# Optimization experiments

Measured on AMD Instinct MI355X. Metric: run time of the kernel, lower is better.

## Reference

```python
import jax, jax.numpy as jnp
import numpy as np

EPS = 1e-12  # matches F.normalize eps

def _l2norm(x):
    n = jnp.sqrt(jnp.sum(x * x, axis=-1, keepdims=True))
    return x / jnp.maximum(n, EPS)

def setup_inputs() -> dict:
    key = jax.random.key(0)
    k1, k2, k3, k4 = jax.random.split(key, 4)
    Bq, Lq, H = 32, 32, 768
    ppq = 8
    Bd, Ld = Bq * ppq, 512
    dim = 128
    q_hidden = jax.random.normal(k1, (Bq, Lq, H), dtype=jnp.float32)
    d_hidden = jax.random.normal(k2, (Bd, Ld, H), dtype=jnp.float32)
    W = jax.random.normal(k3, (dim, H), dtype=jnp.float32) * (1.0 / np.sqrt(H))
    d_mask = jax.random.randint(k4, (Bd, Ld), 0, 2).astype(bool)
    d_mask = d_mask.at[:, 0].set(True)  # guarantee >=1 valid token per doc
    return {"q_hidden": q_hidden, "d_hidden": d_hidden, "W": W,
            "d_mask": d_mask, "ppq": ppq}

def reference(q_hidden, d_hidden, W, d_mask, ppq):
    # linear projection (no bias) + L2 normalize, as in query()/doc()
    q = _l2norm(jnp.einsum('bqh,dh->bqd', q_hidden, W))        # [Bq, Lq, dim]
    d = _l2norm(jnp.einsum('bkh,dh->bkd', d_hidden, W))        # [Bd, Ld, dim]
    d = d * d_mask[..., None].astype(d.dtype)                  # zero masked tokens
    qd = jnp.repeat(q, ppq, axis=0)                            # [Bd, Lq, dim]
    sim = jnp.einsum('bqd,bkd->bqk', qd, d)                    # cosine MaxSim scores
    sim = jnp.where(d_mask[:, None, :], sim, -jnp.inf)         # mask doc tokens
    return jnp.sum(jnp.max(sim, axis=-1), axis=-1)             # [Bd]
```

## Files before the change

kernel.cpp:

```cpp
#include <hip/hip_runtime.h>
#include <math.h>

#define H    768
#define NT   24
#define DIM  128
#define LQ   32
#define LD   512
#define BM   256
#define EPSF 1e-12f

typedef _Float16 f16x8 __attribute__((ext_vector_type(8)));
typedef _Float16 f16x4 __attribute__((ext_vector_type(4)));
typedef float    f32x4 __attribute__((ext_vector_type(4)));

static __device__ __forceinline__ unsigned short h2u(_Float16 h) {
    return __builtin_bit_cast(unsigned short, h);
}

#define GLOAD_LDS16(g, l) __builtin_amdgcn_global_load_lds(                    \
    (const __attribute__((address_space(1))) unsigned int*)(const void*)(g),   \
    (__attribute__((address_space(3))) unsigned int*)(void*)(l), 16, 0, 0)

__global__ __launch_bounds__(256) void wconv_kernel(
    const float* __restrict__ W, unsigned short* __restrict__ wsW,
    float* __restrict__ WT)
{
    const int ks  = blockIdx.x;
    const int tid = threadIdx.x;
    #pragma unroll 4
    for (int i = 0; i < 16; ++i) {
        const int idx = tid + i * 256;
        const int row = idx >> 5, col = idx & 31;
        const float x = W[(size_t)row * H + ks * 32 + col];
        const _Float16 hi = (_Float16)x;
        const _Float16 lo = (_Float16)(x - (float)hi);
        const int colS = (((col >> 3) ^ ((row >> 1) & 3)) << 3) | (col & 7);
        wsW[(((size_t)ks * 2 + 0) * 128 + row) * 32 + colS] = h2u(hi);
        wsW[(((size_t)ks * 2 + 1) * 128 + row) * 32 + colS] = h2u(lo);
        WT[((size_t)ks * 32 + col) * DIM + row] = x;
    }
}

__global__ __launch_bounds__(128) void qproj_kernel(
    const float* __restrict__ qh, const float* __restrict__ WT,
    unsigned short* __restrict__ qn)
{
    const int blk = blockIdx.x;
    const int tid = threadIdx.x;
    __shared__ float rows[4][H];
    __shared__ float red[128];

    const float4* src = (const float4*)(qh + (size_t)blk * 4 * H);
    float4*       dst = (float4*)&rows[0][0];
    for (int i = tid; i < 4 * H / 4; i += 128) dst[i] = src[i];
    __syncthreads();

    float acc[4] = {0.f, 0.f, 0.f, 0.f};
    #pragma unroll 8
    for (int h = 0; h < H; ++h) {
        const float wv = WT[(size_t)h * DIM + tid];
        acc[0] += wv * rows[0][h];
        acc[1] += wv * rows[1][h];
        acc[2] += wv * rows[2][h];
        acc[3] += wv * rows[3][h];
    }
    #pragma unroll
    for (int j = 0; j < 4; ++j) {
        red[tid] = acc[j] * acc[j];
        __syncthreads();
        for (int s = 64; s > 0; s >>= 1) {
            if (tid < s) red[tid] += red[tid + s];
            __syncthreads();
        }
        const float inv = 1.0f / fmaxf(sqrtf(red[0]), EPSF);
        qn[((size_t)blk * 4 + j) * DIM + tid] = h2u((_Float16)(acc[j] * inv));
        __syncthreads();
    }
}

struct Smem {
    union {
        struct {
            unsigned short A[2][BM][32];
            unsigned short Wt[2][2][128][32];
        } g;
        unsigned short C[BM][DIM];
    } u;
    float         pnorm[2][BM];
    unsigned char mk[BM];
    float         pmax[LQ][8];
};

__global__ __launch_bounds__(512, 4) void docgemm_kernel(
    const float* __restrict__ dh, const unsigned short* __restrict__ wsW,
    const int* __restrict__ dmask, const unsigned short* __restrict__ qn,
    float* __restrict__ part, const int* __restrict__ ppq_p)
{
    __shared__ Smem sm;
    const int blk = blockIdx.x;
    const int b   = blk >> 1;
    const int c   = blk & 1;
    const int tid = threadIdx.x;
    const int w   = tid >> 6;
    const int wm  = w >> 1, wn = w & 1;
    const int l   = tid & 63;
    const int g   = l >> 4;
    const int r15 = l & 15;
    const int ppq = ppq_p[0];

    const int r0   = tid >> 3;
    const int seg0 = tid & 7;
    const int aswz = (r0 >> 1) & 3;
    const int coli = (((seg0 >> 1) ^ aswz) << 3) | ((seg0 & 1) << 2);

    const float* Abase = dh + ((size_t)b * LD + (size_t)c * BM) * H;

    f32x4 acc[4][4];
    #pragma unroll
    for (int m = 0; m < 4; ++m)
        #pragma unroll
        for (int n = 0; n < 4; ++n)
            acc[m][n] = (f32x4){0.f, 0.f, 0.f, 0.f};

    float4 avA[4];

    {
        const char* wt   = (const char*)wsW;
        char*       wdst = (char*)&sm.u.g.Wt[0][0][0][0];
        GLOAD_LDS16(wt + tid * 16,        wdst + (w * 64) * 16);
        GLOAD_LDS16(wt + 8192 + tid * 16, wdst + 8192 + (w * 64) * 16);
        __builtin_amdgcn_sched_barrier(0);
        #pragma unroll
        for (int i = 0; i < 4; ++i)
            avA[i] = *(const float4*)(Abase + (size_t)(r0 + i * 64) * H + seg0 * 4);
        #pragma unroll
        for (int i = 0; i < 4; ++i) {
            const int row = r0 + i * 64;
            f16x4 h;
            h[0] = (_Float16)avA[i].x; h[1] = (_Float16)avA[i].y;
            h[2] = (_Float16)avA[i].z; h[3] = (_Float16)avA[i].w;
            *(f16x4*)&sm.u.g.A[0][row][coli] = h;
        }
        #pragma unroll
        for (int i = 0; i < 4; ++i)
            avA[i] = *(const float4*)(Abase + (size_t)(r0 + i * 64) * H + 32 + seg0 * 4);
        asm volatile("s_waitcnt vmcnt(4) lgkmcnt(0)" ::: "memory");
        __builtin_amdgcn_sched_barrier(0);
        __builtin_amdgcn_s_barrier();
        __builtin_amdgcn_sched_barrier(0);
    }

    for (int t = 0; t < NT; ++t) {
        const int cur = t & 1, nxt = cur ^ 1;

        if (t + 1 < NT) {
            const char* wt   = (const char*)wsW + (size_t)(t + 1) * 16384;
            char*       wdst = (char*)&sm.u.g.Wt[nxt][0][0][0];
            GLOAD_LDS16(wt + tid * 16,        wdst + (w * 64) * 16);
            GLOAD_LDS16(wt + 8192 + tid * 16, wdst + 8192 + (w * 64) * 16);
        }
        __builtin_amdgcn_sched_barrier(0);

        f16x8 ah[4];
        #pragma unroll
        for (int m = 0; m < 4; ++m) {
            const int row = wm * 64 + m * 16 + r15;
            const int sl  = (g ^ ((row >> 1) & 3)) * 8;
            ah[m] = *(const f16x8*)&sm.u.g.A[cur][row][sl];
        }
        __builtin_amdgcn_s_setprio(1);
        #pragma unroll
        for (int n = 0; n < 4; ++n) {
            const int row = wn * 64 + n * 16 + r15;
            const int sl  = (g ^ ((row >> 1) & 3)) * 8;
            f16x8 bh = *(const f16x8*)&sm.u.g.Wt[cur][0][row][sl];
            f16x8 bl = *(const f16x8*)&sm.u.g.Wt[cur][1][row][sl];
            #pragma unroll
            for (int m = 0; m < 4; ++m)
                acc[m][n] = __builtin_amdgcn_mfma_f32_16x16x32_f16(ah[m], bh, acc[m][n], 0, 0, 0);
            #pragma unroll
            for (int m = 0; m < 4; ++m)
                acc[m][n] = __builtin_amdgcn_mfma_f32_16x16x32_f16(ah[m], bl, acc[m][n], 0, 0, 0);
        }
        __builtin_amdgcn_s_setprio(0);

        if (t + 1 < NT) {
            #pragma unroll
            for (int i = 0; i < 4; ++i) {
                const int row = r0 + i * 64;
                f16x4 h;
                h[0] = (_Float16)avA[i].x; h[1] = (_Float16)avA[i].y;
                h[2] = (_Float16)avA[i].z; h[3] = (_Float16)avA[i].w;
                *(f16x4*)&sm.u.g.A[nxt][row][coli] = h;
            }
        }
        if (t + 2 < NT) {
            const int k0n = (t + 2) * 32;
            #pragma unroll
            for (int i = 0; i < 4; ++i)
                avA[i] = *(const float4*)(Abase + (size_t)(r0 + i * 64) * H + k0n + seg0 * 4);
        }

        if (t + 2 < NT) {
            asm volatile("s_waitcnt vmcnt(4) lgkmcnt(0)" ::: "memory");
        } else {
            asm volatile("s_waitcnt vmcnt(0) lgkmcnt(0)" ::: "memory");
        }
        __builtin_amdgcn_sched_barrier(0);
        __builtin_amdgcn_s_barrier();
        __builtin_amdgcn_sched_barrier(0);
    }

    #pragma unroll
    for (int m = 0; m < 4; ++m) {
        const int tokb = wm * 64 + m * 16 + g * 4;
        #pragma unroll
        for (int n = 0; n < 4; ++n) {
            const int dim = wn * 64 + n * 16 + r15;
            #pragma unroll
            for (int r = 0; r < 4; ++r) {
                const int tok  = tokb + r;
                const int slot = (dim >> 3) ^ (tok & 7);
                sm.u.C[tok][slot * 8 + (dim & 7)] = h2u((_Float16)acc[m][n][r]);
            }
        }
    }
    #pragma unroll
    for (int m = 0; m < 4; ++m) {
        #pragma unroll
        for (int r = 0; r < 4; ++r) {
            float s = 0.f;
            #pragma unroll
            for (int n = 0; n < 4; ++n) s += acc[m][n][r] * acc[m][n][r];
            s += __shfl_xor(s, 1); s += __shfl_xor(s, 2);
            s += __shfl_xor(s, 4); s += __shfl_xor(s, 8);
            if (r15 == 0) sm.pnorm[wn][wm * 64 + m * 16 + g * 4 + r] = s;
        }
    }
    if (tid < BM) sm.mk[tid] = (unsigned char)(dmask[(size_t)b * LD + c * BM + tid] != 0);
    __syncthreads();

    const unsigned short* qb = qn + (size_t)(b / ppq) * LQ * DIM;
    const int t0 = w * 32 + r15, t1 = t0 + 16;
    const float inv0 = 1.0f / fmaxf(sqrtf(sm.pnorm[0][t0] + sm.pnorm[1][t0]), EPSF);
    const float inv1 = 1.0f / fmaxf(sqrtf(sm.pnorm[0][t1] + sm.pnorm[1][t1]), EPSF);

    f32x4 sacc[2][2];
    #pragma unroll
    for (int m = 0; m < 2; ++m)
        #pragma unroll
        for (int n = 0; n < 2; ++n)
            sacc[m][n] = (f32x4){0.f, 0.f, 0.f, 0.f};
    #pragma unroll
    for (int ks = 0; ks < 4; ++ks) {
        f16x8 qa[2], cb[2];
        #pragma unroll
        for (int m = 0; m < 2; ++m)
            qa[m] = *(const f16x8*)(qb + (size_t)(m * 16 + r15) * DIM + ks * 32 + g * 8);
        #pragma unroll
        for (int n = 0; n < 2; ++n) {
            const int row  = w * 32 + n * 16 + r15;
            const int slot = (ks * 4 + g) ^ (row & 7);
            cb[n] = *(const f16x8*)&sm.u.C[row][slot * 8];
        }
        #pragma unroll
        for (int m = 0; m < 2; ++m)
            #pragma unroll
            for (int n = 0; n < 2; ++n)
                sacc[m][n] = __builtin_amdgcn_mfma_f32_16x16x32_f16(qa[m], cb[n], sacc[m][n], 0, 0, 0);
    }

    const int m0 = sm.mk[t0], m1 = sm.mk[t1];
    #pragma unroll
    for (int m = 0; m < 2; ++m) {
        #pragma unroll
        for (int r = 0; r < 4; ++r) {
            float v0 = m0 ? sacc[m][0][r] * inv0 : -INFINITY;
            float v1 = m1 ? sacc[m][1][r] * inv1 : -INFINITY;
            float vmax = fmaxf(v0, v1);
            vmax = fmaxf(vmax, __shfl_xor(vmax, 1));
            vmax = fmaxf(vmax, __shfl_xor(vmax, 2));
            vmax = fmaxf(vmax, __shfl_xor(vmax, 4));
            vmax = fmaxf(vmax, __shfl_xor(vmax, 8));
            if (r15 == 0) sm.pmax[m * 16 + g * 4 + r][w] = vmax;
        }
    }
    __syncthreads();
    if (tid < LQ) {
        float mv = sm.pmax[tid][0];
        #pragma unroll
        for (int j = 1; j < 8; ++j) mv = fmaxf(mv, sm.pmax[tid][j]);
        part[(size_t)blk * 32 + tid] = mv;
    }
}

__global__ __launch_bounds__(64) void final_kernel(
    const float* __restrict__ part, float* __restrict__ out)
{
    const int b = blockIdx.x;
    const int q = threadIdx.x & 31;
    const float* p = part + (size_t)b * 64;
    float m = fmaxf(p[q], p[32 + q]);
    #pragma unroll
    for (int off = 1; off < 32; off <<= 1) m += __shfl_xor(m, off);
    if (threadIdx.x == 0) out[b] = m;
}

extern "C" void kernel_launch(void* const* d_in, const int* in_sizes, int n_in,
                              void* d_out, int out_size, void* d_ws, size_t ws_size,
                              hipStream_t stream) {
    const float* qh    = (const float*)d_in[0];
    const float* dh    = (const float*)d_in[1];
    const float* W     = (const float*)d_in[2];
    const int*   dmask = (const int*)d_in[3];
    const int*   ppq   = (const int*)d_in[4];
    float*       out   = (float*)d_out;

    unsigned short* wsW  = (unsigned short*)d_ws;
    float*          WT   = (float*)((char*)d_ws + 393216);
    unsigned short* qn   = (unsigned short*)((char*)d_ws + 786432);
    float*          part = (float*)((char*)d_ws + 1048576);

    const int nq = in_sizes[0] / H;
    const int Bd = out_size;

    wconv_kernel<<<NT, 256, 0, stream>>>(W, wsW, WT);
    qproj_kernel<<<nq / 4, 128, 0, stream>>>(qh, WT, qn);
    docgemm_kernel<<<Bd * 2, 512, 0, stream>>>(dh, wsW, dmask, qn, part, ppq);
    final_kernel<<<Bd, 64, 0, stream>>>(part, out);
}
```

Baseline: 147.9 us.

## Drop the fp16 low-part correction for W and halve the doc tile

W is now stored as a single fp16 value instead of an fp16 hi/lo split. This halves the W staging buffer, the LDS B reads and the MFMA count per k-step. The doc GEMM tile also shrinks from 256 to 128 rows with 256 threads per block, so four blocks per document instead of two and more blocks in flight. The final reduction now combines four partial maxima per query token. The cost is lower projection precision, since the W rounding error is no longer compensated.

```diff
diff --git a/kernel.cpp b/kernel.cpp
--- a/kernel.cpp
+++ b/kernel.cpp
@@ -6,7 +6,7 @@
 #define DIM  128
 #define LQ   32
 #define LD   512
-#define BM   256
+#define BM   128
 #define EPSF 1e-12f
 
 typedef _Float16 f16x8 __attribute__((ext_vector_type(8)));
@@ -32,11 +32,8 @@
         const int idx = tid + i * 256;
         const int row = idx >> 5, col = idx & 31;
         const float x = W[(size_t)row * H + ks * 32 + col];
-        const _Float16 hi = (_Float16)x;
-        const _Float16 lo = (_Float16)(x - (float)hi);
         const int colS = (((col >> 3) ^ ((row >> 1) & 3)) << 3) | (col & 7);
-        wsW[(((size_t)ks * 2 + 0) * 128 + row) * 32 + colS] = h2u(hi);
-        wsW[(((size_t)ks * 2 + 1) * 128 + row) * 32 + colS] = h2u(lo);
+        wsW[((size_t)ks * 128 + row) * 32 + colS] = h2u((_Float16)x);
         WT[((size_t)ks * 32 + col) * DIM + row] = x;
     }
 }
@@ -82,24 +79,24 @@
     union {
         struct {
             unsigned short A[2][BM][32];
-            unsigned short Wt[2][2][128][32];
+            unsigned short Wt[2][128][32];
         } g;
         unsigned short C[BM][DIM];
     } u;
     float         pnorm[2][BM];
     unsigned char mk[BM];
-    float         pmax[LQ][8];
+    float         pmax[LQ][4];
 };
 
-__global__ __launch_bounds__(512, 4) void docgemm_kernel(
+__global__ __launch_bounds__(256, 4) void docgemm_kernel(
     const float* __restrict__ dh, const unsigned short* __restrict__ wsW,
     const int* __restrict__ dmask, const unsigned short* __restrict__ qn,
     float* __restrict__ part, const int* __restrict__ ppq_p)
 {
     __shared__ Smem sm;
     const int blk = blockIdx.x;
-    const int b   = blk >> 1;
-    const int c   = blk & 1;
+    const int b   = blk >> 2;
+    const int c   = blk & 3;
     const int tid = threadIdx.x;
     const int w   = tid >> 6;
     const int wm  = w >> 1, wn = w & 1;
@@ -126,16 +123,16 @@
 
     {
         const char* wt   = (const char*)wsW;
-        char*       wdst = (char*)&sm.u.g.Wt[0][0][0][0];
-        GLOAD_LDS16(wt + tid * 16,        wdst + (w * 64) * 16);
-        GLOAD_LDS16(wt + 8192 + tid * 16, wdst + 8192 + (w * 64) * 16);
+        char*       wdst = (char*)&sm.u.g.Wt[0][0][0];
+        GLOAD_LDS16(wt + tid * 16,        wdst + w * 1024);
+        GLOAD_LDS16(wt + 4096 + tid * 16, wdst + 4096 + w * 1024);
         __builtin_amdgcn_sched_barrier(0);
         #pragma unroll
         for (int i = 0; i < 4; ++i)
-            avA[i] = *(const float4*)(Abase + (size_t)(r0 + i * 64) * H + seg0 * 4);
+            avA[i] = *(const float4*)(Abase + (size_t)(r0 + i * 32) * H + seg0 * 4);
         #pragma unroll
         for (int i = 0; i < 4; ++i) {
-            const int row = r0 + i * 64;
+            const int row = r0 + i * 32;
             f16x4 h;
             h[0] = (_Float16)avA[i].x; h[1] = (_Float16)avA[i].y;
             h[2] = (_Float16)avA[i].z; h[3] = (_Float16)avA[i].w;
@@ -143,7 +140,7 @@
         }
         #pragma unroll
         for (int i = 0; i < 4; ++i)
-            avA[i] = *(const float4*)(Abase + (size_t)(r0 + i * 64) * H + 32 + seg0 * 4);
+            avA[i] = *(const float4*)(Abase + (size_t)(r0 + i * 32) * H + 32 + seg0 * 4);
         asm volatile("s_waitcnt vmcnt(4) lgkmcnt(0)" ::: "memory");
         __builtin_amdgcn_sched_barrier(0);
         __builtin_amdgcn_s_barrier();
@@ -154,10 +151,10 @@
         const int cur = t & 1, nxt = cur ^ 1;
 
         if (t + 1 < NT) {
-            const char* wt   = (const char*)wsW + (size_t)(t + 1) * 16384;
-            char*       wdst = (char*)&sm.u.g.Wt[nxt][0][0][0];
-            GLOAD_LDS16(wt + tid * 16,        wdst + (w * 64) * 16);
-            GLOAD_LDS16(wt + 8192 + tid * 16, wdst + 8192 + (w * 64) * 16);
+            const char* wt   = (const char*)wsW + (size_t)(t + 1) * 8192;
+            char*       wdst = (char*)&sm.u.g.Wt[nxt][0][0];
+            GLOAD_LDS16(wt + tid * 16,        wdst + w * 1024);
+            GLOAD_LDS16(wt + 4096 + tid * 16, wdst + 4096 + w * 1024);
         }
         __builtin_amdgcn_sched_barrier(0);
 
@@ -173,21 +170,17 @@
         for (int n = 0; n < 4; ++n) {
             const int row = wn * 64 + n * 16 + r15;
             const int sl  = (g ^ ((row >> 1) & 3)) * 8;
-            f16x8 bh = *(const f16x8*)&sm.u.g.Wt[cur][0][row][sl];
-            f16x8 bl = *(const f16x8*)&sm.u.g.Wt[cur][1][row][sl];
+            f16x8 bh = *(const f16x8*)&sm.u.g.Wt[cur][row][sl];
             #pragma unroll
             for (int m = 0; m < 4; ++m)
                 acc[m][n] = __builtin_amdgcn_mfma_f32_16x16x32_f16(ah[m], bh, acc[m][n], 0, 0, 0);
-            #pragma unroll
-            for (int m = 0; m < 4; ++m)
-                acc[m][n] = __builtin_amdgcn_mfma_f32_16x16x32_f16(ah[m], bl, acc[m][n], 0, 0, 0);
         }
         __builtin_amdgcn_s_setprio(0);
 
         if (t + 1 < NT) {
             #pragma unroll
             for (int i = 0; i < 4; ++i) {
-                const int row = r0 + i * 64;
+                const int row = r0 + i * 32;
                 f16x4 h;
                 h[0] = (_Float16)avA[i].x; h[1] = (_Float16)avA[i].y;
                 h[2] = (_Float16)avA[i].z; h[3] = (_Float16)avA[i].w;
@@ -198,7 +191,7 @@
             const int k0n = (t + 2) * 32;
             #pragma unroll
             for (int i = 0; i < 4; ++i)
-                avA[i] = *(const float4*)(Abase + (size_t)(r0 + i * 64) * H + k0n + seg0 * 4);
+                avA[i] = *(const float4*)(Abase + (size_t)(r0 + i * 32) * H + k0n + seg0 * 4);
         }
 
         if (t + 2 < NT) {
@@ -287,9 +280,8 @@
     }
     __syncthreads();
     if (tid < LQ) {
-        float mv = sm.pmax[tid][0];
-        #pragma unroll
-        for (int j = 1; j < 8; ++j) mv = fmaxf(mv, sm.pmax[tid][j]);
+        float mv = fmaxf(fmaxf(sm.pmax[tid][0], sm.pmax[tid][1]),
+                         fmaxf(sm.pmax[tid][2], sm.pmax[tid][3]));
         part[(size_t)blk * 32 + tid] = mv;
     }
 }
@@ -299,8 +291,8 @@
 {
     const int b = blockIdx.x;
     const int q = threadIdx.x & 31;
-    const float* p = part + (size_t)b * 64;
-    float m = fmaxf(p[q], p[32 + q]);
+    const float* p = part + (size_t)b * 128;
+    float m = fmaxf(fmaxf(p[q], p[32 + q]), fmaxf(p[64 + q], p[96 + q]));
     #pragma unroll
     for (int off = 1; off < 32; off <<= 1) m += __shfl_xor(m, off);
     if (threadIdx.x == 0) out[b] = m;
@@ -317,15 +309,15 @@
     float*       out   = (float*)d_out;
 
     unsigned short* wsW  = (unsigned short*)d_ws;
-    float*          WT   = (float*)((char*)d_ws + 393216);
-    unsigned short* qn   = (unsigned short*)((char*)d_ws + 786432);
-    float*          part = (float*)((char*)d_ws + 1048576);
+    float*          WT   = (float*)((char*)d_ws + 196608);
+    unsigned short* qn   = (unsigned short*)((char*)d_ws + 589824);
+    float*          part = (float*)((char*)d_ws + 851968);
 
     const int nq = in_sizes[0] / H;
     const int Bd = out_size;
 
     wconv_kernel<<<NT, 256, 0, stream>>>(W, wsW, WT);
     qproj_kernel<<<nq / 4, 128, 0, stream>>>(qh, WT, qn);
-    docgemm_kernel<<<Bd * 2, 512, 0, stream>>>(dh, wsW, dmask, qn, part, ppq);
+    docgemm_kernel<<<Bd * 4, 256, 0, stream>>>(dh, wsW, dmask, qn, part, ppq);
     final_kernel<<<Bd, 64, 0, stream>>>(part, out);
 }
```

Measured after the change: 131.5 us. -11.1%, faster.
